# Performance work log

Hardware: AMD Instinct MI355X
Metric: run time of the kernel (lower is better)

## Reference

```python
import jax, jax.numpy as jnp
import numpy as np

VOL_SIZE = 1.0  # config.render.volume_size


def _make_grid(G, vol_size):
    # pytorch3d Volumes.get_coord_grid(world_coordinates=True): axis-aligned grid
    # centered at origin, spacing = voxel_size = vol_size/G, last dim is (x,y,z)
    # with x varying along W, y along H, z along D.
    m = (G - 1) / 2.0 * (vol_size / G)
    lin = jnp.linspace(-m, m, G, dtype=jnp.float32)
    zz, yy, xx = jnp.meshgrid(lin, lin, lin, indexing='ij')
    return jnp.stack([xx, yy, zz], axis=-1)  # [G,G,G,3]


def _grid_sample_3d(vol, grid):
    # vol: [N,C,D,H,W]; grid: [N,Dg,Hg,Wg,3] xyz in [-1,1].
    # Matches torch F.grid_sample(mode='bilinear', padding_mode='zeros', align_corners=False).
    N, C, D, H, W = vol.shape
    ix = ((grid[..., 0] + 1.0) * W - 1.0) * 0.5
    iy = ((grid[..., 1] + 1.0) * H - 1.0) * 0.5
    iz = ((grid[..., 2] + 1.0) * D - 1.0) * 0.5
    x0f, y0f, z0f = jnp.floor(ix), jnp.floor(iy), jnp.floor(iz)
    tx, ty, tz = ix - x0f, iy - y0f, iz - z0f
    x0, y0, z0 = x0f.astype(jnp.int32), y0f.astype(jnp.int32), z0f.astype(jnp.int32)

    def per_batch(v, z0, y0, x0, tx, ty, tz):
        # v: [C,D,H,W]; index/weight maps: [Dg,Hg,Wg]
        def corner(z, y, x):
            valid = (z >= 0) & (z < D) & (y >= 0) & (y < H) & (x >= 0) & (x < W)
            zc = jnp.clip(z, 0, D - 1)
            yc = jnp.clip(y, 0, H - 1)
            xc = jnp.clip(x, 0, W - 1)
            return v[:, zc, yc, xc] * valid[None]  # [C,Dg,Hg,Wg]
        z1, y1, x1 = z0 + 1, y0 + 1, x0 + 1
        acc = jnp.zeros((C,) + z0.shape, dtype=v.dtype)
        for zc, wz in ((z0, 1.0 - tz), (z1, tz)):
            for yc, wy in ((y0, 1.0 - ty), (y1, ty)):
                for xc, wx in ((x0, 1.0 - tx), (x1, tx)):
                    acc = acc + corner(zc, yc, xc) * (wz * wy * wx)[None]
        return acc

    return jax.vmap(per_batch)(vol, z0, y0, x0, tx, ty, tz)


def reference(voxels, camPoses_cv2, grid_size):
    B, t, C, D, H, W = voxels.shape
    G = grid_size
    m = (G - 1) / 2.0 * (VOL_SIZE / G)  # grid_coord_max
    grid_coord = _make_grid(G, VOL_SIZE)  # [G,G,G,3]

    # T = pose_0 @ pose_1^{-1}, per (B, t-1) pair
    pose0 = jnp.broadcast_to(camPoses_cv2[:, 0:1], (B, t - 1, 4, 4)).reshape(B * (t - 1), 4, 4)
    pose1 = camPoses_cv2[:, 1:].reshape(B * (t - 1), 4, 4)
    T = pose0 @ jnp.linalg.inv(pose1)

    # homogeneous transform of world grid points: cam = R @ p + trans
    pts = grid_coord.reshape(-1, 3)  # [N=G^3, 3]
    R, trans = T[:, :3, :3], T[:, :3, 3]
    cam = jnp.einsum('nij,pj->npi', R, pts) + trans[:, None, :]  # [B*(t-1), N, 3]
    sample_grid = (cam / m).reshape(B * (t - 1), D, H, W, 3)

    warped = _grid_sample_3d(voxels[:, 1:].reshape(B * (t - 1), C, D, H, W), sample_grid)
    out = jnp.concatenate([voxels[:, 0:1], warped.reshape(B, t - 1, C, D, H, W)], axis=1)
    return out


def setup_inputs() -> dict:
    key = jax.random.key(0)
    kv, ka, kt = jax.random.split(key, 3)
    B, t, C, G = 2, 5, 16, 64
    voxels = jax.random.normal(kv, (B, t, C, G, G, G), dtype=jnp.float32)
    # build valid SE(3)-ish camera poses (orthonormal rotation + small translation)
    A = jax.random.normal(ka, (B, t, 3, 3), dtype=jnp.float32)
    Q, _ = jnp.linalg.qr(A)
    det = jnp.linalg.det(Q)
    Q = Q * jnp.sign(det)[..., None, None]  # ensure det=+1
    trans = 0.2 * jax.random.normal(kt, (B, t, 3), dtype=jnp.float32)
    top = jnp.concatenate([Q, trans[..., None]], axis=-1)  # [B,t,3,4]
    bottom = jnp.broadcast_to(jnp.array([0.0, 0.0, 0.0, 1.0], jnp.float32), (B, t, 1, 4))
    camPoses_cv2 = jnp.concatenate([top, bottom], axis=-2)  # [B,t,4,4]
    return {"voxels": voxels, "camPoses_cv2": camPoses_cv2, "grid_size": G}
```

## Files before the change

kernel.cpp:

```cpp
#include <hip/hip_runtime.h>

#define G3_    (64 * 64 * 64)
#define CCH    16
#define TT     5
#define LSTRIDE 17
#define BUF    4096
#define NCHB   2
#define NWARP  (4096 * (CCH / NCHB))
#define NCOPY  8192
#define NBLK   (NWARP + NCOPY)


__global__ void coeff_kernel(const float* __restrict__ cam, float* __restrict__ Tc)
{
    int n = threadIdx.x;
    if (n >= 8) return;
    int b = n >> 2, j = n & 3;
    const float* p0 = cam + (size_t)(b * TT) * 16;
    const float* p1 = cam + (size_t)(b * TT + j + 1) * 16;
    float a00 = p0[0], a01 = p0[1], a02 = p0[2],  at0 = p0[3];
    float a10 = p0[4], a11 = p0[5], a12 = p0[6],  at1 = p0[7];
    float a20 = p0[8], a21 = p0[9], a22 = p0[10], at2 = p0[11];
    float b00 = p1[0], b01 = p1[1], b02 = p1[2],  bt0 = p1[3];
    float b10 = p1[4], b11 = p1[5], b12 = p1[6],  bt1 = p1[7];
    float b20 = p1[8], b21 = p1[9], b22 = p1[10], bt2 = p1[11];
    float R00 = a00*b00 + a01*b01 + a02*b02;
    float R01 = a00*b10 + a01*b11 + a02*b12;
    float R02 = a00*b20 + a01*b21 + a02*b22;
    float R10 = a10*b00 + a11*b01 + a12*b02;
    float R11 = a10*b10 + a11*b11 + a12*b12;
    float R12 = a10*b20 + a11*b21 + a12*b22;
    float R20 = a20*b00 + a21*b01 + a22*b02;
    float R21 = a20*b10 + a21*b11 + a22*b12;
    float R22 = a20*b20 + a21*b21 + a22*b22;
    float trx = at0 - (R00*bt0 + R01*bt1 + R02*bt2);
    float try_= at1 - (R10*bt0 + R11*bt1 + R12*bt2);
    float trz = at2 - (R20*bt0 + R21*bt1 + R22*bt2);

    const float S  = 1.0f / 64.0f;
    const float SC = 32.0f / 0.4921875f;
    float ax = SC * R00 * S, bx = SC * R01 * S, cx = SC * R02 * S;
    float ay = SC * R10 * S, by = SC * R11 * S, cy = SC * R12 * S;
    float az = SC * R20 * S, bz = SC * R21 * S, cz = SC * R22 * S;
    float* o = Tc + n * 12;
    o[0] = ax; o[1] = bx; o[2] = cx;
    o[3] = ay; o[4] = by; o[5] = cy;
    o[6] = az; o[7] = bz; o[8] = cz;
    o[9]  = -31.5f * (ax + bx + cx) + SC * trx + 31.5f;
    o[10] = -31.5f * (ay + by + cy) + SC * try_ + 31.5f;
    o[11] = -31.5f * (az + bz + cz) + SC * trz + 31.5f;
}

__global__ __launch_bounds__(256) void fused_kernel(const float* __restrict__ vox,
                                                    const float* __restrict__ Tc,
                                                    float* __restrict__ out)
{
    __shared__ float lds[BUF];
    const int tid = threadIdx.x;

    const int bid  = blockIdx.x;
    const int sbid = (bid & 7) * (NBLK / 8) + (bid >> 3);
    const int q5   = sbid / 5;
    const int r5   = sbid - q5 * 5;

    if (r5 == 4) {
        int t4 = q5 * 256 + tid;
        int b  = t4 >> 20;
        int rr = t4 & ((1 << 20) - 1);
        size_t base = (size_t)(b * TT) * CCH * G3_;
        const float4* s = (const float4*)(vox + base);
        float4* d = (float4*)(out + base);
        d[rr] = s[rr];
        return;
    }

    const int wid = q5 * 4 + r5;
    const int cg  = wid >> 12;
    const int t9  = wid & 4095;
    const int n   = t9 >> 9;
    const int t6  = t9 & 511;
    const int ox  = (t6 & 7) << 3;
    const int oy  = ((t6 >> 3) & 7) << 3;
    const int oz  = (t6 >> 6) << 3;
    const int b   = n >> 2, j = n & 3;

    const float* Cp = Tc + n * 12;
    const float ax = Cp[0], bx = Cp[1], cx = Cp[2];
    const float ay = Cp[3], by = Cp[4], cy = Cp[5];
    const float az = Cp[6], bz = Cp[7], cz = Cp[8];
    const float kx = Cp[9], ky = Cp[10], kz = Cp[11];

    float x0a = ax * ox, x0b = ax * (ox + 7);
    float x1a = bx * oy, x1b = bx * (oy + 7);
    float x2a = cx * oz, x2b = cx * (oz + 7);
    float min_ix = kx + fminf(x0a, x0b) + fminf(x1a, x1b) + fminf(x2a, x2b);
    float max_ix = kx + fmaxf(x0a, x0b) + fmaxf(x1a, x1b) + fmaxf(x2a, x2b);
    float y0a = ay * ox, y0b = ay * (ox + 7);
    float y1a = by * oy, y1b = by * (oy + 7);
    float y2a = cy * oz, y2b = cy * (oz + 7);
    float min_iy = ky + fminf(y0a, y0b) + fminf(y1a, y1b) + fminf(y2a, y2b);
    float max_iy = ky + fmaxf(y0a, y0b) + fmaxf(y1a, y1b) + fmaxf(y2a, y2b);
    float z0a = az * ox, z0b = az * (ox + 7);
    float z1a = bz * oy, z1b = bz * (oy + 7);
    float z2a = cz * oz, z2b = cz * (oz + 7);
    float min_iz = kz + fminf(z0a, z0b) + fminf(z1a, z1b) + fminf(z2a, z2b);
    float max_iz = kz + fmaxf(z0a, z0b) + fmaxf(z1a, z1b) + fmaxf(z2a, z2b);

    int xlo = min(max((int)floorf(min_ix), 0), 63);
    int xhi = min(max((int)floorf(max_ix) + 1, 0), 63);
    int ylo = min(max((int)floorf(min_iy), 0), 63);
    int yhi = min(max((int)floorf(max_iy) + 1, 0), 63);
    int zlo = min(max((int)floorf(min_iz), 0), 63);
    int zhi = min(max((int)floorf(max_iz) + 1, 0), 63);
    const int xlo_e = xlo & ~1;
    const int sxe = xhi - xlo_e + 1;
    const int sy  = yhi - ylo + 1;
    const int sz  = zhi - zlo + 1;
    const int lstep = sy * LSTRIDE;

    const int gx0 = ox + ((tid & 3) << 1);
    const int gy  = oy + ((tid >> 2) & 7);
    const int gz  = oz + (tid >> 5);
    const float ix0 = kx + ax * gx0 + bx * gy + cx * gz;
    const float iy0 = ky + ay * gx0 + by * gy + cy * gz;
    const float iz0 = kz + az * gx0 + bz * gy + cz * gz;

    float wx0[2], wx1[2], wy0[2], wy1[2], wz0[2], wz1[2];
    int base0[2], base1[2];
    #pragma unroll
    for (int k = 0; k < 2; ++k) {
        float ix = ix0 + (k ? ax : 0.0f);
        float iy = iy0 + (k ? ay : 0.0f);
        float iz = iz0 + (k ? az : 0.0f);
        float fx = floorf(ix), fy = floorf(iy), fz = floorf(iz);
        float tx = ix - fx, ty = iy - fy, tz = iz - fz;
        int X0 = (int)fx, Y0 = (int)fy, Z0 = (int)fz;

        float w0 = ((unsigned)X0 < 64u) ? (1.0f - tx) : 0.0f;
        float w1 = ((unsigned)(X0 + 1) < 64u) ? tx : 0.0f;
        int rxu = X0 - xlo_e;
        wx0[k] = (rxu < 0) ? w1 : w0;
        wx1[k] = (rxu < 0) ? 0.0f : w1;
        int rx0 = min(max(rxu, 0), sxe - 1);

        w0 = ((unsigned)Y0 < 64u) ? (1.0f - ty) : 0.0f;
        w1 = ((unsigned)(Y0 + 1) < 64u) ? ty : 0.0f;
        int ryu = Y0 - ylo;
        wy0[k] = (ryu < 0) ? w1 : w0;
        wy1[k] = (ryu < 0) ? 0.0f : w1;
        int ry0 = min(max(ryu, 0), sy - 1);

        wz0[k] = ((unsigned)Z0 < 64u) ? (1.0f - tz) : 0.0f;
        wz1[k] = ((unsigned)(Z0 + 1) < 64u) ? tz : 0.0f;
        int rz0 = min(max(Z0     - zlo, 0), sz - 1);
        int rz1 = min(max(Z0 + 1 - zlo, 0), sz - 1);

        base0[k] = rz0 * lstep + ry0 * LSTRIDE + rx0;
        base1[k] = rz1 * lstep + ry0 * LSTRIDE + rx0;
    }
    const int soff = (gz << 12) + (gy << 6) + gx0;

    const size_t fb = ((size_t)(b * TT + j + 1) * CCH + cg * NCHB) * G3_;
    const float* vbase = vox + fb;
    float* obase = out + fb;

    const int lane8 = tid & 7;
    const int row16 = (tid >> 3) & 15;
    const int zh    = tid >> 7;
    const int xe    = xlo_e + (lane8 << 1);
    const bool actS = (xe <= xhi) && (row16 < sy);
    const int grow  = (zlo << 12) + ((ylo + row16) << 6) + xe;
    const int lrow  = row16 * LSTRIDE + (lane8 << 1);

    float2 stg[8];

    if (actS) {
        const float2* gp = (const float2*)(vbase + grow);
        #pragma unroll
        for (int k = 0; k < 8; ++k) {
            int zz = (k << 1) + zh;
            if (zz < sz) stg[k] = gp[(size_t)zz << 11];
        }
    }

    {
        int rz = tid >> 4, ry = tid & 15;
        if (rz < sz && ry < sy) lds[rz * lstep + ry * LSTRIDE + sxe] = 0.0f;
        if (tid < 17) lds[sz * lstep + tid] = 0.0f;
    }
    if (actS) {
        #pragma unroll
        for (int k = 0; k < 8; ++k) {
            int zz = (k << 1) + zh;
            if (zz < sz) {
                float* wp = lds + lrow + zz * lstep;
                wp[0] = stg[k].x;
                wp[1] = stg[k].y;
            }
        }
    }
    __syncthreads();

    #pragma unroll
    for (int cc = 0; cc < NCHB; ++cc) {
        const bool pre = (cc + 1 < NCHB);
        if (pre && actS) {
            const float2* gp = (const float2*)(vbase + (size_t)(cc + 1) * G3_ + grow);
            #pragma unroll
            for (int k = 0; k < 8; ++k) {
                int zz = (k << 1) + zh;
                if (zz < sz) stg[k] = gp[(size_t)zz << 11];
            }
        }

        float* op = obase + (size_t)cc * G3_;
        float res[2];
        #pragma unroll
        for (int k = 0; k < 2; ++k) {
            const float* pz0 = lds + base0[k];
            const float* pz1 = lds + base1[k];
            float v000 = pz0[0],  v001 = pz0[1];
            float v010 = pz0[17], v011 = pz0[18];
            float v100 = pz1[0],  v101 = pz1[1];
            float v110 = pz1[17], v111 = pz1[18];
            float t00 = v000 * wx0[k] + v001 * wx1[k];
            float t01 = v010 * wx0[k] + v011 * wx1[k];
            float t10 = v100 * wx0[k] + v101 * wx1[k];
            float t11 = v110 * wx0[k] + v111 * wx1[k];
            float u0  = t00 * wy0[k] + t01 * wy1[k];
            float u1  = t10 * wy0[k] + t11 * wy1[k];
            res[k] = u0 * wz0[k] + u1 * wz1[k];
        }
        *(float2*)(op + soff) = make_float2(res[0], res[1]);

        if (pre) {
            __syncthreads();
            if (actS) {
                #pragma unroll
                for (int k = 0; k < 8; ++k) {
                    int zz = (k << 1) + zh;
                    if (zz < sz) {
                        float* wp = lds + lrow + zz * lstep;
                        wp[0] = stg[k].x;
                        wp[1] = stg[k].y;
                    }
                }
            }
            __syncthreads();
        }
    }
}

extern "C" void kernel_launch(void* const* d_in, const int* in_sizes, int n_in,
                              void* d_out, int out_size, void* d_ws, size_t ws_size,
                              hipStream_t stream)
{
    const float* vox = (const float*)d_in[0];
    const float* cam = (const float*)d_in[1];
    float* out = (float*)d_out;
    float* Tc  = (float*)d_ws;

    hipLaunchKernelGGL(coeff_kernel, dim3(1), dim3(64), 0, stream, cam, Tc);
    hipLaunchKernelGGL(fused_kernel, dim3(NBLK), dim3(256), 0, stream, vox, Tc, out);
}
```

Before: 344.8 us.

## Process one channel per block and precompute tile bounding boxes in a table

Each warp block now handles a single channel instead of two, doubling the block count and dropping the in-block prefetch/double-buffer loop and its extra barriers. The copy-to-warp block interleave ratio changes from 1:4 to 1:8 to match. A new small kernel precomputes each tile's source bounding box into a packed table in workspace so warp blocks load one word instead of recomputing the bbox. This trades per-block setup and staging overhead (repeated per channel now) for more parallelism and fewer syncs.

```diff
diff --git a/kernel.cpp b/kernel.cpp
--- a/kernel.cpp
+++ b/kernel.cpp
@@ -5,8 +5,7 @@
 #define TT     5
 #define LSTRIDE 17
 #define BUF    4096
-#define NCHB   2
-#define NWARP  (4096 * (CCH / NCHB))
+#define NWARP  65536
 #define NCOPY  8192
 #define NBLK   (NWARP + NCOPY)
 
@@ -51,40 +50,10 @@
     o[11] = -31.5f * (az + bz + cz) + SC * trz + 31.5f;
 }
 
-__global__ __launch_bounds__(256) void fused_kernel(const float* __restrict__ vox,
-                                                    const float* __restrict__ Tc,
-                                                    float* __restrict__ out)
-{
-    __shared__ float lds[BUF];
-    const int tid = threadIdx.x;
-
-    const int bid  = blockIdx.x;
-    const int sbid = (bid & 7) * (NBLK / 8) + (bid >> 3);
-    const int q5   = sbid / 5;
-    const int r5   = sbid - q5 * 5;
-
-    if (r5 == 4) {
-        int t4 = q5 * 256 + tid;
-        int b  = t4 >> 20;
-        int rr = t4 & ((1 << 20) - 1);
-        size_t base = (size_t)(b * TT) * CCH * G3_;
-        const float4* s = (const float4*)(vox + base);
-        float4* d = (float4*)(out + base);
-        d[rr] = s[rr];
-        return;
-    }
-
-    const int wid = q5 * 4 + r5;
-    const int cg  = wid >> 12;
-    const int t9  = wid & 4095;
-    const int n   = t9 >> 9;
-    const int t6  = t9 & 511;
-    const int ox  = (t6 & 7) << 3;
-    const int oy  = ((t6 >> 3) & 7) << 3;
-    const int oz  = (t6 >> 6) << 3;
-    const int b   = n >> 2, j = n & 3;
-
-    const float* Cp = Tc + n * 12;
+__device__ __forceinline__ void tile_bbox(const float* Cp, int ox, int oy, int oz,
+                                          int& xlo_e, int& ylo, int& zlo,
+                                          int& sxe, int& sy, int& sz)
+{
     const float ax = Cp[0], bx = Cp[1], cx = Cp[2];
     const float ay = Cp[3], by = Cp[4], cy = Cp[5];
     const float az = Cp[6], bz = Cp[7], cz = Cp[8];
@@ -108,14 +77,83 @@
 
     int xlo = min(max((int)floorf(min_ix), 0), 63);
     int xhi = min(max((int)floorf(max_ix) + 1, 0), 63);
-    int ylo = min(max((int)floorf(min_iy), 0), 63);
+    ylo     = min(max((int)floorf(min_iy), 0), 63);
     int yhi = min(max((int)floorf(max_iy) + 1, 0), 63);
-    int zlo = min(max((int)floorf(min_iz), 0), 63);
+    zlo     = min(max((int)floorf(min_iz), 0), 63);
     int zhi = min(max((int)floorf(max_iz) + 1, 0), 63);
-    const int xlo_e = xlo & ~1;
-    const int sxe = xhi - xlo_e + 1;
-    const int sy  = yhi - ylo + 1;
-    const int sz  = zhi - zlo + 1;
+    xlo_e = xlo & ~1;
+    sxe   = xhi - xlo_e + 1;
+    sy    = yhi - ylo + 1;
+    sz    = zhi - zlo + 1;
+}
+
+__global__ void bbox_kernel(const float* __restrict__ Tc, unsigned* __restrict__ Bb)
+{
+    int t9 = blockIdx.x * 256 + threadIdx.x;
+    if (t9 >= 4096) return;
+    int n  = t9 >> 9;
+    int t6 = t9 & 511;
+    int ox = (t6 & 7) << 3, oy = ((t6 >> 3) & 7) << 3, oz = (t6 >> 6) << 3;
+    int xlo_e, ylo, zlo, sxe, sy, sz;
+    tile_bbox(Tc + n * 12, ox, oy, oz, xlo_e, ylo, zlo, sxe, sy, sz);
+    Bb[t9] = (unsigned)xlo_e | ((unsigned)ylo << 6) | ((unsigned)zlo << 12)
+           | ((unsigned)sxe << 18) | ((unsigned)sy << 23) | ((unsigned)sz << 27);
+}
+
+template<bool TBL>
+__global__ __launch_bounds__(256) void fused_kernel(const float* __restrict__ vox,
+                                                    const float* __restrict__ Tc,
+                                                    const unsigned* __restrict__ Bb,
+                                                    float* __restrict__ out)
+{
+    __shared__ float lds[BUF];
+    const int tid = threadIdx.x;
+
+    const int bid  = blockIdx.x;
+    const int sbid = (bid & 7) * (NBLK / 8) + (bid >> 3);
+    const int q9   = sbid / 9;
+    const int r9   = sbid - q9 * 9;
+
+    if (r9 == 8) {
+        int t4 = q9 * 256 + tid;
+        int b  = t4 >> 20;
+        int rr = t4 & ((1 << 20) - 1);
+        size_t base = (size_t)(b * TT) * CCH * G3_;
+        const float4* s = (const float4*)(vox + base);
+        float4* d = (float4*)(out + base);
+        d[rr] = s[rr];
+        return;
+    }
+
+    const int wid = q9 * 8 + r9;
+    const int cg  = wid >> 12;
+    const int t9  = wid & 4095;
+    const int n   = t9 >> 9;
+    const int t6  = t9 & 511;
+    const int ox  = (t6 & 7) << 3;
+    const int oy  = ((t6 >> 3) & 7) << 3;
+    const int oz  = (t6 >> 6) << 3;
+    const int b   = n >> 2, j = n & 3;
+
+    const float* Cp = Tc + n * 12;
+    const float ax = Cp[0], bx = Cp[1], cx = Cp[2];
+    const float ay = Cp[3], by = Cp[4], cy = Cp[5];
+    const float az = Cp[6], bz = Cp[7], cz = Cp[8];
+    const float kx = Cp[9], ky = Cp[10], kz = Cp[11];
+
+    int xlo_e, ylo, zlo, sxe, sy, sz;
+    if (TBL) {
+        unsigned u = Bb[t9];
+        xlo_e = u & 63;
+        ylo   = (u >> 6) & 63;
+        zlo   = (u >> 12) & 63;
+        sxe   = (u >> 18) & 31;
+        sy    = (u >> 23) & 15;
+        sz    = (u >> 27) & 15;
+    } else {
+        tile_bbox(Cp, ox, oy, oz, xlo_e, ylo, zlo, sxe, sy, sz);
+    }
+    const int xhi   = xlo_e + sxe - 1;
     const int lstep = sy * LSTRIDE;
 
     const int gx0 = ox + ((tid & 3) << 1);
@@ -160,9 +198,8 @@
     }
     const int soff = (gz << 12) + (gy << 6) + gx0;
 
-    const size_t fb = ((size_t)(b * TT + j + 1) * CCH + cg * NCHB) * G3_;
+    const size_t fb = ((size_t)(b * TT + j + 1) * CCH + cg) * G3_;
     const float* vbase = vox + fb;
-    float* obase = out + fb;
 
     const int lane8 = tid & 7;
     const int row16 = (tid >> 3) & 15;
@@ -182,7 +219,6 @@
             if (zz < sz) stg[k] = gp[(size_t)zz << 11];
         }
     }
-
     {
         int rz = tid >> 4, ry = tid & 15;
         if (rz < sz && ry < sy) lds[rz * lstep + ry * LSTRIDE + sxe] = 0.0f;
@@ -201,54 +237,25 @@
     }
     __syncthreads();
 
+    float* op = out + fb;
+    float res[2];
     #pragma unroll
-    for (int cc = 0; cc < NCHB; ++cc) {
-        const bool pre = (cc + 1 < NCHB);
-        if (pre && actS) {
-            const float2* gp = (const float2*)(vbase + (size_t)(cc + 1) * G3_ + grow);
-            #pragma unroll
-            for (int k = 0; k < 8; ++k) {
-                int zz = (k << 1) + zh;
-                if (zz < sz) stg[k] = gp[(size_t)zz << 11];
-            }
-        }
-
-        float* op = obase + (size_t)cc * G3_;
-        float res[2];
-        #pragma unroll
-        for (int k = 0; k < 2; ++k) {
-            const float* pz0 = lds + base0[k];
-            const float* pz1 = lds + base1[k];
-            float v000 = pz0[0],  v001 = pz0[1];
-            float v010 = pz0[17], v011 = pz0[18];
-            float v100 = pz1[0],  v101 = pz1[1];
-            float v110 = pz1[17], v111 = pz1[18];
-            float t00 = v000 * wx0[k] + v001 * wx1[k];
-            float t01 = v010 * wx0[k] + v011 * wx1[k];
-            float t10 = v100 * wx0[k] + v101 * wx1[k];
-            float t11 = v110 * wx0[k] + v111 * wx1[k];
-            float u0  = t00 * wy0[k] + t01 * wy1[k];
-            float u1  = t10 * wy0[k] + t11 * wy1[k];
-            res[k] = u0 * wz0[k] + u1 * wz1[k];
-        }
-        *(float2*)(op + soff) = make_float2(res[0], res[1]);
-
-        if (pre) {
-            __syncthreads();
-            if (actS) {
-                #pragma unroll
-                for (int k = 0; k < 8; ++k) {
-                    int zz = (k << 1) + zh;
-                    if (zz < sz) {
-                        float* wp = lds + lrow + zz * lstep;
-                        wp[0] = stg[k].x;
-                        wp[1] = stg[k].y;
-                    }
-                }
-            }
-            __syncthreads();
-        }
-    }
+    for (int k = 0; k < 2; ++k) {
+        const float* pz0 = lds + base0[k];
+        const float* pz1 = lds + base1[k];
+        float v000 = pz0[0],  v001 = pz0[1];
+        float v010 = pz0[17], v011 = pz0[18];
+        float v100 = pz1[0],  v101 = pz1[1];
+        float v110 = pz1[17], v111 = pz1[18];
+        float t00 = v000 * wx0[k] + v001 * wx1[k];
+        float t01 = v010 * wx0[k] + v011 * wx1[k];
+        float t10 = v100 * wx0[k] + v101 * wx1[k];
+        float t11 = v110 * wx0[k] + v111 * wx1[k];
+        float u0  = t00 * wy0[k] + t01 * wy1[k];
+        float u1  = t10 * wy0[k] + t11 * wy1[k];
+        res[k] = u0 * wz0[k] + u1 * wz1[k];
+    }
+    *(float2*)(op + soff) = make_float2(res[0], res[1]);
 }
 
 extern "C" void kernel_launch(void* const* d_in, const int* in_sizes, int n_in,
@@ -259,7 +266,15 @@
     const float* cam = (const float*)d_in[1];
     float* out = (float*)d_out;
     float* Tc  = (float*)d_ws;
+    unsigned* Bb = (unsigned*)((char*)d_ws + 512);
 
     hipLaunchKernelGGL(coeff_kernel, dim3(1), dim3(64), 0, stream, cam, Tc);
-    hipLaunchKernelGGL(fused_kernel, dim3(NBLK), dim3(256), 0, stream, vox, Tc, out);
-}
+    if (ws_size >= 512 + 4096 * sizeof(unsigned)) {
+        hipLaunchKernelGGL(bbox_kernel, dim3(16), dim3(256), 0, stream, Tc, Bb);
+        hipLaunchKernelGGL((fused_kernel<true>), dim3(NBLK), dim3(256), 0, stream,
+                           vox, Tc, Bb, out);
+    } else {
+        hipLaunchKernelGGL((fused_kernel<false>), dim3(NBLK), dim3(256), 0, stream,
+                           vox, Tc, (const unsigned*)nullptr, out);
+    }
+}
```

After: 339.3 us. About the same (-1.6%).
